# Performance work log

Measured on AMD Instinct MI355X. Metric: run time of the kernel, lower is better.

The kernel has to match this reference:

```python
import jax, jax.numpy as jnp
import numpy as np
from jax import lax

NUM_CLASSES = 19
BINS_NUM = 51
LOSS_WEIGHT = 1.0


def setup_inputs() -> dict:
    key = jax.random.key(0)
    k1, k2 = jax.random.split(key)
    feature = jax.random.normal(k1, (1, 256, 64, 64), dtype=jnp.float32)
    label = jax.random.randint(k2, (1, 1, 64, 64), 0, NUM_CLASSES).astype(jnp.int64)
    return {"feature": feature, "label": label}


def reference(feature, label):
    # feature: [1, D, H, W]; label: [1, 1, H, W] (same spatial size -> nearest resize is identity)
    D = feature.shape[1]
    C = NUM_CLASSES
    F = feature[0].reshape(D, -1).T            # [N, D] pixel feature vectors
    L = label[0, 0].reshape(-1).astype(jnp.int32)  # [N] class id per pixel

    counts = jax.ops.segment_sum(jnp.ones(L.shape, jnp.float32), L, num_segments=C)  # [C]
    sum_f = jax.ops.segment_sum(F, L, num_segments=C)        # [C, D]
    sum_f2 = jax.ops.segment_sum(F * F, L, num_segments=C)   # [C, D]
    has = counts > 0
    cnt = jnp.maximum(counts, 1.0)
    miu = sum_f / cnt[:, None]                                # first-iter: direct assignment (no EMA yet)
    moment2 = sum_f2 / cnt[:, None]
    var = jnp.maximum(moment2 - miu ** 2, 1e-12)
    # stats are computed via detached numpy in the original -> no grad
    miu = lax.stop_gradient(miu)
    var = lax.stop_gradient(var)
    var_sample = var / 25.0

    bins = jnp.linspace(-5.0, 5.0, BINS_NUM).astype(jnp.float32)  # [B]

    # target gaussian pdf per (class, feature-dim, bin): [C, D, B]
    inv_norm_t = 1.0 / jnp.sqrt(2.0 * jnp.pi * var)
    target = jnp.exp(-0.5 * (bins[None, None, :] - miu[:, :, None]) ** 2 / var[:, :, None]) * inv_norm_t[:, :, None]

    # sample KDE per pixel, scatter-added into its class: [N, D, B] -> [C, D, B]
    vs_p = var_sample[L]                                      # [N, D]
    inv_norm_s = 1.0 / jnp.sqrt(2.0 * jnp.pi * vs_p)          # [N, D]
    K = jnp.exp(-0.5 * (bins[None, None, :] - F[:, :, None]) ** 2 / vs_p[:, :, None]) * inv_norm_s[:, :, None]
    samp = jax.ops.segment_sum(K, L, num_segments=C)          # [C, D, B]

    samp_den = jnp.where(has[:, None], jnp.maximum(samp.sum(-1), 1e-30), 1.0)[:, :, None]
    tgt_den = jnp.where(has[:, None], jnp.maximum(target.sum(-1), 1e-30), 1.0)[:, :, None]
    hist = samp / samp_den
    target = target / tgt_den

    # smooth L1 (beta=1, mean reduction) per class
    diff = hist - target
    ad = jnp.abs(diff)
    sl1 = jnp.where(ad < 1.0, 0.5 * diff * diff, ad - 0.5).mean(axis=(1, 2))  # [C]

    active = has & (jnp.arange(C) > 0)
    active_num = jnp.sum(active.astype(jnp.float32))
    loss = jnp.sum(jnp.where(active, sl1, 0.0)) / (active_num + 1e-12)
    return (LOSS_WEIGHT * loss, feature)
```

## Files before the change

### kernel.cpp

```cpp
#include <hip/hip_runtime.h>

#define N_PIX 4096
#define N_D   256
#define N_C   19
#define N_B   51

#define OFF_LIST   0
#define OFF_COUNTS 311296
#define OFF_ACC    311424

__global__ __launch_bounds__(256) void k_bucket(const int* __restrict__ label,
                                                int* __restrict__ list,
                                                int* __restrict__ counts,
                                                float* __restrict__ acc) {
    const int c = blockIdx.x;
    const int w = threadIdx.x >> 6;
    const int lane = threadIdx.x & 63;
    __shared__ int wcnt[4];
    if (c == 0 && threadIdx.x == 0) *acc = 0.f;

    const int q0 = w * 1024;
    int cnt = 0;
    for (int base = 0; base < 1024; base += 64) {
        const bool match = (label[q0 + base + lane] == c);
        cnt += (int)__popcll(__ballot(match));
    }
    if (lane == 0) wcnt[w] = cnt;
    __syncthreads();
    int m = 0;
#pragma unroll
    for (int i = 0; i < 4; ++i) m += (i < w) ? wcnt[i] : 0;

    for (int base = 0; base < 1024; base += 64) {
        const int n = q0 + base + lane;
        const bool match = (label[n] == c);
        const unsigned long long mask = __ballot(match);
        if (match) list[c * N_PIX + m + __popcll(mask & ((1ull << lane) - 1ull))] = n;
        m += (int)__popcll(mask);
    }
    if (w == 3 && lane == 0) counts[c] = m;
}

__global__ __launch_bounds__(256) void k_main(const float* __restrict__ feature,
                                              const int* __restrict__ list,
                                              const int* __restrict__ counts,
                                              float* __restrict__ acc) {
    const int c = blockIdx.x + 1;
    const int w = threadIdx.x >> 6;
    const int d = blockIdx.y * 4 + w;
    const int lane = threadIdx.x & 63;
    const int m = counts[c];
    __shared__ float blk[4];
    float part = 0.f;
    if (m > 0) {
        const float* __restrict__ row = feature + d * N_PIX;
        const int* __restrict__ lst = list + c * N_PIX;

        float s1 = 0.f, s2 = 0.f;
        for (int j = lane; j < m; j += 64) {
            const float f = row[lst[j]];
            s1 += f;
            s2 += f * f;
        }
#pragma unroll
        for (int off = 32; off; off >>= 1) {
            s1 += __shfl_xor(s1, off);
            s2 += __shfl_xor(s2, off);
        }
        const float cnt = (float)m;
        const float mu = s1 / cnt;
        const float v = fmaxf(s2 / cnt - mu * mu, 1e-12f);

        const float LOG2E = 1.44269504088896340736f;
        const float as = -12.5f * LOG2E / v;
        const float at = -0.5f * LOG2E / v;
        const float bin = (lane < N_B) ? fmaf(0.2f, (float)lane, -5.0f) : 1e18f;
        const float tt = bin - mu;
        const float targ = __builtin_amdgcn_exp2f(at * tt * tt);

        float acc_s = 0.f;
        for (int base = 0; base < m; base += 64) {
            const int j = base + lane;
            const float fl = (j < m) ? row[lst[j]] : -1e18f;
#pragma unroll
            for (int k = 0; k < 64; ++k) {
                const float f = __shfl(fl, k);
                const float t = f - bin;
                acc_s += __builtin_amdgcn_exp2f(as * t * t);
            }
        }

        float ss = acc_s, st = targ;
#pragma unroll
        for (int off = 32; off; off >>= 1) {
            ss += __shfl_xor(ss, off);
            st += __shfl_xor(st, off);
        }
        const float hist = acc_s / fmaxf(ss, 1e-30f);
        const float tgt  = targ  / fmaxf(st, 1e-30f);
        const float diff = hist - tgt;
        const float ad = fabsf(diff);
        float sl1 = (ad < 1.f) ? 0.5f * diff * diff : ad - 0.5f;
#pragma unroll
        for (int off = 32; off; off >>= 1) sl1 += __shfl_down(sl1, off);
        part = sl1;
    }
    if (lane == 0) blk[w] = part;
    __syncthreads();
    if (threadIdx.x == 0) atomicAdd(acc, blk[0] + blk[1] + blk[2] + blk[3]);
}

__global__ __launch_bounds__(64) void k_final(const int* __restrict__ counts,
                                              const float* __restrict__ acc,
                                              float* __restrict__ out) {
    if (threadIdx.x == 0) {
        int active = 0;
        for (int c = 1; c < N_C; ++c) active += (counts[c] > 0) ? 1 : 0;
        out[0] = (*acc) / (float)(N_D * N_B) / ((float)active + 1e-12f);
    }
}

extern "C" void kernel_launch(void* const* d_in, const int* in_sizes, int n_in,
                              void* d_out, int out_size, void* d_ws, size_t ws_size,
                              hipStream_t stream) {
    const float* feature = (const float*)d_in[0];
    const int* label = (const int*)d_in[1];
    float* out = (float*)d_out;
    char* ws = (char*)d_ws;
    int* list = (int*)(ws + OFF_LIST);
    int* counts = (int*)(ws + OFF_COUNTS);
    float* acc = (float*)(ws + OFF_ACC);

    hipMemcpyAsync(out + 1, feature, (size_t)N_PIX * N_D * sizeof(float),
                   hipMemcpyDeviceToDevice, stream);

    k_bucket<<<N_C, 256, 0, stream>>>(label, list, counts, acc);
    dim3 grid(N_C - 1, N_D / 4);
    k_main<<<grid, 256, 0, stream>>>(feature, list, counts, acc);
    k_final<<<1, 64, 0, stream>>>(counts, acc, out);
}
```

Baseline: 96.97 us.

## Fuse bucketing, feature copy and main loss into one kernel with LDS lists

```diff
diff --git a/kernel.cpp b/kernel.cpp
--- a/kernel.cpp
+++ b/kernel.cpp
@@ -5,71 +5,73 @@
 #define N_C   19
 #define N_B   51
 
-#define OFF_LIST   0
-#define OFF_COUNTS 311296
-#define OFF_ACC    311424
+#define OFF_PART   0
+#define OFF_COUNTS 4608
 
-__global__ __launch_bounds__(256) void k_bucket(const int* __restrict__ label,
-                                                int* __restrict__ list,
-                                                int* __restrict__ counts,
-                                                float* __restrict__ acc) {
-    const int c = blockIdx.x;
+__global__ __launch_bounds__(256) void k_fused(const float* __restrict__ feature,
+                                               const int* __restrict__ label,
+                                               float* __restrict__ out,
+                                               float* __restrict__ part,
+                                               int* __restrict__ counts) {
+    const int c = blockIdx.x + 1;
     const int w = threadIdx.x >> 6;
     const int lane = threadIdx.x & 63;
+    const int d = (blockIdx.y << 2) | w;
+    const int bid = blockIdx.x * 64 + blockIdx.y;
+
+    __shared__ int lst[N_PIX];
     __shared__ int wcnt[4];
-    if (c == 0 && threadIdx.x == 0) *acc = 0.f;
+    __shared__ float blk[4];
 
-    const int q0 = w * 1024;
+    {
+        const int t = bid * 256 + threadIdx.x;
+        for (int i = t; i < N_PIX * N_D; i += 18 * 64 * 256)
+            out[1 + i] = feature[i];
+    }
+
+    int lab[16];
+    const int q0 = w << 10;
+#pragma unroll
+    for (int i = 0; i < 16; ++i) lab[i] = label[q0 + (i << 6) + lane];
+
     int cnt = 0;
-    for (int base = 0; base < 1024; base += 64) {
-        const bool match = (label[q0 + base + lane] == c);
-        cnt += (int)__popcll(__ballot(match));
-    }
+#pragma unroll
+    for (int i = 0; i < 16; ++i) cnt += (int)__popcll(__ballot(lab[i] == c));
     if (lane == 0) wcnt[w] = cnt;
     __syncthreads();
-    int m = 0;
+
+    int off = 0, M = 0;
 #pragma unroll
-    for (int i = 0; i < 4; ++i) m += (i < w) ? wcnt[i] : 0;
+    for (int i = 0; i < 4; ++i) { const int v = wcnt[i]; off += (i < w) ? v : 0; M += v; }
 
-    for (int base = 0; base < 1024; base += 64) {
-        const int n = q0 + base + lane;
-        const bool match = (label[n] == c);
-        const unsigned long long mask = __ballot(match);
-        if (match) list[c * N_PIX + m + __popcll(mask & ((1ull << lane) - 1ull))] = n;
-        m += (int)__popcll(mask);
+#pragma unroll
+    for (int i = 0; i < 16; ++i) {
+        const bool match = (lab[i] == c);
+        const unsigned long long mk = __ballot(match);
+        if (match) lst[off + (int)__popcll(mk & ((1ull << lane) - 1ull))] = q0 + (i << 6) + lane;
+        off += (int)__popcll(mk);
     }
-    if (w == 3 && lane == 0) counts[c] = m;
-}
+    if (threadIdx.x == 0 && blockIdx.y == 0) counts[c] = M;
+    __syncthreads();
 
-__global__ __launch_bounds__(256) void k_main(const float* __restrict__ feature,
-                                              const int* __restrict__ list,
-                                              const int* __restrict__ counts,
-                                              float* __restrict__ acc) {
-    const int c = blockIdx.x + 1;
-    const int w = threadIdx.x >> 6;
-    const int d = blockIdx.y * 4 + w;
-    const int lane = threadIdx.x & 63;
-    const int m = counts[c];
-    __shared__ float blk[4];
-    float part = 0.f;
-    if (m > 0) {
+    float partial = 0.f;
+    if (M > 0) {
         const float* __restrict__ row = feature + d * N_PIX;
-        const int* __restrict__ lst = list + c * N_PIX;
 
         float s1 = 0.f, s2 = 0.f;
-        for (int j = lane; j < m; j += 64) {
+        for (int j = lane; j < M; j += 64) {
             const float f = row[lst[j]];
             s1 += f;
             s2 += f * f;
         }
 #pragma unroll
-        for (int off = 32; off; off >>= 1) {
-            s1 += __shfl_xor(s1, off);
-            s2 += __shfl_xor(s2, off);
+        for (int o = 32; o; o >>= 1) {
+            s1 += __shfl_xor(s1, o);
+            s2 += __shfl_xor(s2, o);
         }
-        const float cnt = (float)m;
-        const float mu = s1 / cnt;
-        const float v = fmaxf(s2 / cnt - mu * mu, 1e-12f);
+        const float cntf = (float)M;
+        const float mu = s1 / cntf;
+        const float v = fmaxf(s2 / cntf - mu * mu, 1e-12f);
 
         const float LOG2E = 1.44269504088896340736f;
         const float as = -12.5f * LOG2E / v;
@@ -79,22 +81,24 @@
         const float targ = __builtin_amdgcn_exp2f(at * tt * tt);
 
         float acc_s = 0.f;
-        for (int base = 0; base < m; base += 64) {
-            const int j = base + lane;
-            const float fl = (j < m) ? row[lst[j]] : -1e18f;
+        float fl = (lane < M) ? row[lst[lane]] : -1e18f;
+        for (int base = 0; base < M; base += 64) {
+            const int jn = base + 64 + lane;
+            const float fn = (jn < M) ? row[lst[jn]] : -1e18f;
 #pragma unroll
             for (int k = 0; k < 64; ++k) {
                 const float f = __shfl(fl, k);
                 const float t = f - bin;
                 acc_s += __builtin_amdgcn_exp2f(as * t * t);
             }
+            fl = fn;
         }
 
         float ss = acc_s, st = targ;
 #pragma unroll
-        for (int off = 32; off; off >>= 1) {
-            ss += __shfl_xor(ss, off);
-            st += __shfl_xor(st, off);
+        for (int o = 32; o; o >>= 1) {
+            ss += __shfl_xor(ss, o);
+            st += __shfl_xor(st, o);
         }
         const float hist = acc_s / fmaxf(ss, 1e-30f);
         const float tgt  = targ  / fmaxf(st, 1e-30f);
@@ -102,21 +106,31 @@
         const float ad = fabsf(diff);
         float sl1 = (ad < 1.f) ? 0.5f * diff * diff : ad - 0.5f;
 #pragma unroll
-        for (int off = 32; off; off >>= 1) sl1 += __shfl_down(sl1, off);
-        part = sl1;
+        for (int o = 32; o; o >>= 1) sl1 += __shfl_down(sl1, o);
+        partial = sl1;
     }
-    if (lane == 0) blk[w] = part;
+    if (lane == 0) blk[w] = partial;
     __syncthreads();
-    if (threadIdx.x == 0) atomicAdd(acc, blk[0] + blk[1] + blk[2] + blk[3]);
+    if (threadIdx.x == 0) part[bid] = blk[0] + blk[1] + blk[2] + blk[3];
 }
 
-__global__ __launch_bounds__(64) void k_final(const int* __restrict__ counts,
-                                              const float* __restrict__ acc,
-                                              float* __restrict__ out) {
+__global__ __launch_bounds__(256) void k_final(const float* __restrict__ part,
+                                               const int* __restrict__ counts,
+                                               float* __restrict__ out) {
+    __shared__ float blk[4];
+    const int w = threadIdx.x >> 6;
+    const int lane = threadIdx.x & 63;
+    float s = 0.f;
+    for (int i = threadIdx.x; i < 18 * 64; i += 256) s += part[i];
+#pragma unroll
+    for (int o = 32; o; o >>= 1) s += __shfl_xor(s, o);
+    if (lane == 0) blk[w] = s;
+    __syncthreads();
     if (threadIdx.x == 0) {
         int active = 0;
-        for (int c = 1; c < N_C; ++c) active += (counts[c] > 0) ? 1 : 0;
-        out[0] = (*acc) / (float)(N_D * N_B) / ((float)active + 1e-12f);
+        for (int cc = 1; cc < N_C; ++cc) active += (counts[cc] > 0) ? 1 : 0;
+        out[0] = (blk[0] + blk[1] + blk[2] + blk[3]) / (float)(N_D * N_B)
+                 / ((float)active + 1e-12f);
     }
 }
 
@@ -127,15 +141,10 @@
     const int* label = (const int*)d_in[1];
     float* out = (float*)d_out;
     char* ws = (char*)d_ws;
-    int* list = (int*)(ws + OFF_LIST);
+    float* part = (float*)(ws + OFF_PART);
     int* counts = (int*)(ws + OFF_COUNTS);
-    float* acc = (float*)(ws + OFF_ACC);
 
-    hipMemcpyAsync(out + 1, feature, (size_t)N_PIX * N_D * sizeof(float),
-                   hipMemcpyDeviceToDevice, stream);
-
-    k_bucket<<<N_C, 256, 0, stream>>>(label, list, counts, acc);
     dim3 grid(N_C - 1, N_D / 4);
-    k_main<<<grid, 256, 0, stream>>>(feature, list, counts, acc);
-    k_final<<<1, 64, 0, stream>>>(counts, acc, out);
+    k_fused<<<grid, 256, 0, stream>>>(feature, label, out, part, counts);
+    k_final<<<1, 256, 0, stream>>>(part, counts, out);
 }
```

After: 86.68 us. 10.6% less time.
